# Optimization experiments

Measured on AMD Instinct MI355X. Metric: run time of the kernel, lower is better.

## Reference

```python
import jax, jax.numpy as jnp
import numpy as np

OUT_FEATURES = 4096
IN_FEATURES = 4096
GROUP_SIZE = 256
NUM_GROUPS = OUT_FEATURES * IN_FEATURES // GROUP_SIZE  # 65536


def setup_inputs() -> dict:
    key = jax.random.key(0)
    k1, k2, k3 = jax.random.split(key, 3)
    x = jax.random.normal(k1, (4, 2048, IN_FEATURES), dtype=jnp.float32)
    weight_packed = jax.random.randint(k2, (NUM_GROUPS, GROUP_SIZE // 2), 0, 256, dtype=jnp.int32)
    # params[..., 0] = scale, params[..., 1] = zero_point; keep scales small like real quant params
    weight_params = jax.random.uniform(k3, (NUM_GROUPS, 2), dtype=jnp.float32) * jnp.array([0.01, 0.1], dtype=jnp.float32)
    return {"x": x, "weight_packed": weight_packed, "weight_params": weight_params}


def _dequantize_4bit(weight_packed, weight_params):
    # weight_packed: [G, gs/2] bytes, two 4-bit values per byte (low nibble = even index)
    scales = weight_params[:, 0:1]  # [G, 1]
    zeros = weight_params[:, 1:2]   # [G, 1]
    low = (weight_packed & 15).astype(jnp.float32)          # even positions
    high = ((weight_packed >> 4) & 15).astype(jnp.float32)  # odd positions
    q = jnp.stack([low, high], axis=-1).reshape(weight_packed.shape[0], -1)  # [G, gs]
    return q * scales + zeros


def reference(x, weight_packed, weight_params):
    w = _dequantize_4bit(weight_packed, weight_params)  # [G, gs]
    w = w.reshape(-1)[: OUT_FEATURES * IN_FEATURES].reshape(OUT_FEATURES, IN_FEATURES)
    # F.linear(x, W) = x @ W.T
    return jnp.einsum("bsi,oi->bso", x, w)
```

## Files before the change

### kernel.cpp

```cpp
#include <hip/hip_runtime.h>
#include <hip/hip_bf16.h>


#define M_DIM 8192
#define N_DIM 4096
#define K_DIM 4096

typedef __bf16 bf16x8 __attribute__((ext_vector_type(8)));
typedef float f32x4 __attribute__((ext_vector_type(4)));
typedef unsigned short us8 __attribute__((ext_vector_type(8)));

__device__ __forceinline__ unsigned short f2bf_rne(float f) {
    unsigned int u = __builtin_bit_cast(unsigned int, f);
    u += 0x7FFFu + ((u >> 16) & 1u);
    return (unsigned short)(u >> 16);
}

__global__ void prep_kernel(const float* __restrict__ x,
                            const int* __restrict__ packed,
                            const float* __restrict__ params,
                            ushort* __restrict__ a,
                            ushort* __restrict__ w) {
    int b = blockIdx.x;
    if (b < 16384) {
        int j = b * 256 + threadIdx.x;
        float4 v0 = ((const float4*)x)[2 * j];
        float4 v1 = ((const float4*)x)[2 * j + 1];
        us8 o;
        o[0] = f2bf_rne(v0.x); o[1] = f2bf_rne(v0.y);
        o[2] = f2bf_rne(v0.z); o[3] = f2bf_rne(v0.w);
        o[4] = f2bf_rne(v1.x); o[5] = f2bf_rne(v1.y);
        o[6] = f2bf_rne(v1.z); o[7] = f2bf_rne(v1.w);
        ((us8*)a)[j] = o;
    } else {
        int j = (b - 16384) * 256 + threadIdx.x;
        int4 v = ((const int4*)packed)[j];
        int g = j >> 5;
        float s = params[2 * g], z = params[2 * g + 1];
        unsigned int o0, o1, o2, o3;
        o0 = (unsigned int)f2bf_rne((float)(v.x & 15) * s + z)
           | ((unsigned int)f2bf_rne((float)((v.x >> 4) & 15) * s + z) << 16);
        o1 = (unsigned int)f2bf_rne((float)(v.y & 15) * s + z)
           | ((unsigned int)f2bf_rne((float)((v.y >> 4) & 15) * s + z) << 16);
        o2 = (unsigned int)f2bf_rne((float)(v.z & 15) * s + z)
           | ((unsigned int)f2bf_rne((float)((v.z >> 4) & 15) * s + z) << 16);
        o3 = (unsigned int)f2bf_rne((float)(v.w & 15) * s + z)
           | ((unsigned int)f2bf_rne((float)((v.w >> 4) & 15) * s + z) << 16);
        ((uint4*)w)[j] = make_uint4(o0, o1, o2, o3);
    }
}

__global__ __launch_bounds__(512, 2) void gemm_bt(const ushort* __restrict__ A,
                                                  const ushort* __restrict__ B,
                                                  float* __restrict__ C) {
    __shared__ ushort lds[65536];

    const int tid  = threadIdx.x;
    const int w    = tid >> 6;
    const int lane = tid & 63;
    const int quad = lane >> 4;
    const int l16  = lane & 15;
    const int wm   = w >> 2;
    const int wn   = w & 3;

    const int bid = blockIdx.x;
    const int sid = (bid & 7) * 64 + (bid >> 3);
    const int by  = sid & 31;
    const int bx  = sid >> 5;
    const int m0  = by * 256;
    const int n0  = bx * 256;

    const int srow = tid >> 3;
    const int scol = ((tid & 7) ^ (srow & 7)) * 8;
    const ushort* aS = A + (size_t)(m0 + srow) * K_DIM + scol;
    const ushort* bS = B + (size_t)(n0 + srow) * K_DIM + scol;

    f32x4 acc[8][4] = {};

    auto stageA = [&](int t, int h) {
        const int kc   = (t < 64 ? t : 63) * 64;
        const int slot = ((t & 1) * 2 + h) * 8192;
#pragma unroll
        for (int l = 0; l < 2; ++l)
            __builtin_amdgcn_global_load_lds(
                (const __attribute__((address_space(1))) void*)(aS + (size_t)(h * 128 + l * 64) * K_DIM + kc),
                (__attribute__((address_space(3))) void*)(lds + slot + (l * 512 + w * 64) * 8),
                16, 0, 0);
    };
    auto stageB = [&](int t, int h) {
        const int kc   = (t < 64 ? t : 63) * 64;
        const int slot = 32768 + ((t & 1) * 2 + h) * 8192;
#pragma unroll
        for (int l = 0; l < 2; ++l)
            __builtin_amdgcn_global_load_lds(
                (const __attribute__((address_space(1))) void*)(bS + (size_t)(h * 128 + l * 64) * K_DIM + kc),
                (__attribute__((address_space(3))) void*)(lds + slot + (l * 512 + w * 64) * 8),
                16, 0, 0);
    };

    stageB(0, 0); stageB(0, 1); stageA(0, 0); stageA(0, 1); stageB(1, 0); stageB(1, 1);
    asm volatile("s_waitcnt vmcnt(4)" ::: "memory");
    __builtin_amdgcn_s_barrier();

    const int aBase = wm * 8192;
    const int bBase = 32768 + (wn >> 1) * 8192;
    const int bR0   = (wn & 1) * 64;
    const int swz8  = l16 & 7;

#pragma unroll 1
    for (int i = 0; i < 32; ++i) {
#pragma unroll
        for (int hh = 0; hh < 2; ++hh) {
            const int tc  = 2 * i + hh;
            const int buf = hh * 16384;
            const int sa  = 2 * i + 1 + hh;
            const int sb  = 2 * i + 2 + hh;
            bf16x8 bf[4][2];
#pragma unroll
            for (int q = 0; q < 4; ++q) {
                if (q == 0) {
#pragma unroll
                    for (int j = 0; j < 4; ++j)
#pragma unroll
                        for (int ks = 0; ks < 2; ++ks) {
                            const int r = bR0 + j * 16 + l16;
                            const int c = (ks * 4 + quad) ^ swz8;
                            bf[j][ks] = *(const bf16x8*)&lds[bBase + buf + r * 64 + c * 8];
                        }
                }
                bf16x8 af[2][2];
#pragma unroll
                for (int ii = 0; ii < 2; ++ii)
#pragma unroll
                    for (int ks = 0; ks < 2; ++ks) {
                        const int r = q * 32 + ii * 16 + l16;
                        const int c = (ks * 4 + quad) ^ swz8;
                        af[ii][ks] = *(const bf16x8*)&lds[aBase + buf + r * 64 + c * 8];
                    }
                if (q < 2) stageA(sa, q); else stageB(sb, q - 2);
                if (q == 3) asm volatile("s_waitcnt vmcnt(4)" ::: "memory");
                __builtin_amdgcn_s_barrier();
                __builtin_amdgcn_s_setprio(1);
#pragma unroll
                for (int ks = 0; ks < 2; ++ks)
#pragma unroll
                    for (int ii = 0; ii < 2; ++ii)
#pragma unroll
                        for (int j = 0; j < 4; ++j)
                            acc[q * 2 + ii][j] = __builtin_amdgcn_mfma_f32_16x16x32_bf16(
                                af[ii][ks], bf[j][ks], acc[q * 2 + ii][j], 0, 0, 0);
                __builtin_amdgcn_s_setprio(0);
                __builtin_amdgcn_s_barrier();
            }
        }
    }

    const int crow = m0 + wm * 128 + quad * 4;
    const int ccol = n0 + wn * 64 + l16;
#pragma unroll
    for (int rf = 0; rf < 8; ++rf)
#pragma unroll
        for (int j = 0; j < 4; ++j)
#pragma unroll
            for (int r = 0; r < 4; ++r)
                C[(size_t)(crow + rf * 16 + r) * N_DIM + ccol + j * 16] = acc[rf][j][r];
}

__global__ void naive_kernel(const float* __restrict__ x, const int* __restrict__ packed,
                             const float* __restrict__ params, float* __restrict__ out) {
    int idx = blockIdx.x * blockDim.x + threadIdx.x;
    if (idx >= M_DIM * N_DIM) return;
    int m = idx / N_DIM, o = idx % N_DIM;
    const float* xr = x + (size_t)m * K_DIM;
    float sum = 0.f;
    for (int gi = 0; gi < K_DIM / 256; ++gi) {
        int g = o * (K_DIM / 256) + gi;
        float s = params[2 * g], z = params[2 * g + 1];
        const int* p = packed + (size_t)g * 128;
        const float* xx = xr + gi * 256;
        for (int j = 0; j < 128; ++j) {
            int v = p[j];
            sum += xx[2 * j]     * ((float)(v & 15) * s + z);
            sum += xx[2 * j + 1] * ((float)((v >> 4) & 15) * s + z);
        }
    }
    out[idx] = sum;
}

extern "C" void kernel_launch(void* const* d_in, const int* in_sizes, int n_in,
                              void* d_out, int out_size, void* d_ws, size_t ws_size,
                              hipStream_t stream) {
    const float* x      = (const float*)d_in[0];
    const int*   packed = (const int*)d_in[1];
    const float* params = (const float*)d_in[2];
    float* out = (float*)d_out;

    const size_t a_bytes = (size_t)M_DIM * K_DIM * 2;
    const size_t w_bytes = (size_t)N_DIM * K_DIM * 2;

    if (ws_size >= a_bytes + w_bytes) {
        ushort* Abf = (ushort*)d_ws;
        ushort* Wbf = (ushort*)((char*)d_ws + a_bytes);

        prep_kernel<<<24576, 256, 0, stream>>>(x, packed, params, Abf, Wbf);

        gemm_bt<<<512, 512, 0, stream>>>(Abf, Wbf, out);
    } else {
        int n = M_DIM * N_DIM;
        naive_kernel<<<(n + 255) / 256, 256, 0, stream>>>(x, packed, params, out);
    }
}
```

Measured before the change: 461.1 us.

## Software-pipeline LDS fragment reads with MFMA and cut barriers per k-tile

Restructures the GEMM main loop so LDS fragment reads for the next phase, and for the next tile's first B/A fragments, are issued while the current phase's MFMAs run. A and B fragments are double-buffered in registers. Barriers per tile drop from eight to two, using explicit waitcnt and sched_barrier to keep ordering. The aim is to hide LDS latency and barrier stalls behind matrix math. In exchange it adds register pressure under launch_bounds(512,2) and relies on delicate hazard ordering around buffer reuse.

```diff
diff --git a/kernel.cpp b/kernel.cpp
--- a/kernel.cpp
+++ b/kernel.cpp
@@ -76,6 +76,9 @@
     const ushort* bS = B + (size_t)(n0 + srow) * K_DIM + scol;
 
     f32x4 acc[8][4] = {};
+    bf16x8 afA[2][2], afB[2][2];
+    bf16x8 bf0a[4], bf0b[4];
+    bf16x8 bf1[4];
 
     auto stageA = [&](int t, int h) {
         const int kc   = (t < 64 ? t : 63) * 64;
@@ -98,62 +101,94 @@
                 16, 0, 0);
     };
 
-    stageB(0, 0); stageB(0, 1); stageA(0, 0); stageA(0, 1); stageB(1, 0); stageB(1, 1);
-    asm volatile("s_waitcnt vmcnt(4)" ::: "memory");
-    __builtin_amdgcn_s_barrier();
-
     const int aBase = wm * 8192;
     const int bBase = 32768 + (wn >> 1) * 8192;
     const int bR0   = (wn & 1) * 64;
     const int swz8  = l16 & 7;
 
+    auto readAF = [&](bf16x8 (&dst)[2][2], int buf, int ph) {
+#pragma unroll
+        for (int ii = 0; ii < 2; ++ii)
+#pragma unroll
+            for (int ks = 0; ks < 2; ++ks)
+                dst[ii][ks] = *(const bf16x8*)&lds[aBase + buf +
+                    (ph * 32 + ii * 16 + l16) * 64 + ((ks * 4 + quad) ^ swz8) * 8];
+    };
+    auto readBF0 = [&](bf16x8 (&dst)[4], int buf) {
+#pragma unroll
+        for (int j = 0; j < 4; ++j)
+            dst[j] = *(const bf16x8*)&lds[bBase + buf +
+                (bR0 + j * 16 + l16) * 64 + (quad ^ swz8) * 8];
+    };
+    auto readBF1 = [&](int buf) {
+#pragma unroll
+        for (int j = 0; j < 4; ++j)
+            bf1[j] = *(const bf16x8*)&lds[bBase + buf +
+                (bR0 + j * 16 + l16) * 64 + ((4 + quad) ^ swz8) * 8];
+    };
+
+#define MFMA_PH(PH, AF, BF0)                                                   \
+    do {                                                                       \
+        __builtin_amdgcn_s_setprio(1);                                         \
+        _Pragma("unroll")                                                      \
+        for (int ii = 0; ii < 2; ++ii)                                         \
+            _Pragma("unroll")                                                  \
+            for (int j = 0; j < 4; ++j)                                        \
+                acc[(PH) * 2 + ii][j] = __builtin_amdgcn_mfma_f32_16x16x32_bf16( \
+                    AF[ii][0], BF0[j], acc[(PH) * 2 + ii][j], 0, 0, 0);        \
+        _Pragma("unroll")                                                      \
+        for (int ii = 0; ii < 2; ++ii)                                         \
+            _Pragma("unroll")                                                  \
+            for (int j = 0; j < 4; ++j)                                        \
+                acc[(PH) * 2 + ii][j] = __builtin_amdgcn_mfma_f32_16x16x32_bf16( \
+                    AF[ii][1], bf1[j], acc[(PH) * 2 + ii][j], 0, 0, 0);        \
+        __builtin_amdgcn_s_setprio(0);                                         \
+    } while (0)
+
+    stageB(0, 0); stageB(0, 1); stageA(0, 0); stageA(0, 1); stageB(1, 0); stageB(1, 1);
+    asm volatile("s_waitcnt vmcnt(4)" ::: "memory");
+    __builtin_amdgcn_s_barrier();
+    asm volatile("" ::: "memory");
+    readBF0(bf0a, 0);
+    readAF(afA, 0, 0);
+
+#define TILE(T, BUF, NBUF, BF0C, BF0N)                                         \
+    do {                                                                       \
+        const int t = (T);                                                     \
+                                                                      \
+        readBF1(BUF);                                                          \
+        readAF(afB, BUF, 1);                                                   \
+        stageA(t + 1, 0);                                                      \
+        MFMA_PH(0, afA, BF0C);                                                 \
+                                                                      \
+        readAF(afA, BUF, 2);                                                   \
+        stageA(t + 1, 1);                                                      \
+        MFMA_PH(1, afB, BF0C);                                                 \
+        asm volatile("s_waitcnt lgkmcnt(0)" ::: "memory");                     \
+        __builtin_amdgcn_sched_barrier(0);                                     \
+        __builtin_amdgcn_s_barrier();                 \
+        asm volatile("" ::: "memory");                                         \
+                                                                      \
+        readAF(afB, BUF, 3);                                                   \
+        stageB(t + 2, 0);                                                      \
+        MFMA_PH(2, afA, BF0C);                                                 \
+                                                                      \
+        stageB(t + 2, 1);                                                      \
+        asm volatile("s_waitcnt vmcnt(4) lgkmcnt(0)" ::: "memory");            \
+        __builtin_amdgcn_s_barrier();                \
+        asm volatile("" ::: "memory");                                         \
+        if (t < 63) { readBF0(BF0N, NBUF); readAF(afA, NBUF, 0); }             \
+        __builtin_amdgcn_sched_barrier(0);                                     \
+        MFMA_PH(3, afB, BF0C);                                                 \
+    } while (0)
+
 #pragma unroll 1
-    for (int i = 0; i < 32; ++i) {
-#pragma unroll
-        for (int hh = 0; hh < 2; ++hh) {
-            const int tc  = 2 * i + hh;
-            const int buf = hh * 16384;
-            const int sa  = 2 * i + 1 + hh;
-            const int sb  = 2 * i + 2 + hh;
-            bf16x8 bf[4][2];
-#pragma unroll
-            for (int q = 0; q < 4; ++q) {
-                if (q == 0) {
-#pragma unroll
-                    for (int j = 0; j < 4; ++j)
-#pragma unroll
-                        for (int ks = 0; ks < 2; ++ks) {
-                            const int r = bR0 + j * 16 + l16;
-                            const int c = (ks * 4 + quad) ^ swz8;
-                            bf[j][ks] = *(const bf16x8*)&lds[bBase + buf + r * 64 + c * 8];
-                        }
-                }
-                bf16x8 af[2][2];
-#pragma unroll
-                for (int ii = 0; ii < 2; ++ii)
-#pragma unroll
-                    for (int ks = 0; ks < 2; ++ks) {
-                        const int r = q * 32 + ii * 16 + l16;
-                        const int c = (ks * 4 + quad) ^ swz8;
-                        af[ii][ks] = *(const bf16x8*)&lds[aBase + buf + r * 64 + c * 8];
-                    }
-                if (q < 2) stageA(sa, q); else stageB(sb, q - 2);
-                if (q == 3) asm volatile("s_waitcnt vmcnt(4)" ::: "memory");
-                __builtin_amdgcn_s_barrier();
-                __builtin_amdgcn_s_setprio(1);
-#pragma unroll
-                for (int ks = 0; ks < 2; ++ks)
-#pragma unroll
-                    for (int ii = 0; ii < 2; ++ii)
-#pragma unroll
-                        for (int j = 0; j < 4; ++j)
-                            acc[q * 2 + ii][j] = __builtin_amdgcn_mfma_f32_16x16x32_bf16(
-                                af[ii][ks], bf[j][ks], acc[q * 2 + ii][j], 0, 0, 0);
-                __builtin_amdgcn_s_setprio(0);
-                __builtin_amdgcn_s_barrier();
-            }
-        }
-    }
+    for (int tt = 0; tt < 64; tt += 2) {
+        TILE(tt,     0,     16384, bf0a, bf0b);
+        TILE(tt + 1, 16384, 0,     bf0b, bf0a);
+    }
+#undef TILE
+#undef MFMA_PH
 
     const int crow = m0 + wm * 128 + quad * 4;
     const int ccol = n0 + wn * 64 + l16;
```

New measurement: 445.2 us. -3.4%, faster.
